# Performance work log

Measured on AMD Instinct MI355X. Metric: run time of the kernel, lower is better.

Reference implementation:

```python
import jax, jax.numpy as jnp
import numpy as np

CURVE = 1.0
TAU = 0.5
N_NODES = 32768
N_EDGES = 65536
IN_CH = 64
OUT_CH = 64
N_HEADS = 8
N_RF = 128
EPS = 1e-7


def _make_projection_matrix(m, d, seed=0):
    # FAVOR+ projection: stacked rows of transposed QR blocks, row-rescaled by chi norms.
    rng = np.random.RandomState(seed)
    blocks = []
    nb_full = m // d
    for _ in range(nb_full):
        q, _ = np.linalg.qr(rng.randn(d, d))
        blocks.append(q.T)
    rem = m - nb_full * d
    if rem > 0:
        q, _ = np.linalg.qr(rng.randn(d, d))
        blocks.append(q.T[:rem])
    final = np.vstack(blocks)  # [m, d]
    mult = np.linalg.norm(rng.randn(m, d), axis=1)
    return (mult[:, None] * final).astype(np.float32)


def _expmap0(u, c):
    # Hyperboloid exp map at origin; time slot of u is ignored.
    sqrtK = 1.0 / jnp.sqrt(c)
    x = u[..., 1:]
    xn = jnp.maximum(jnp.linalg.norm(x, axis=-1, keepdims=True), EPS)
    theta = xn / sqrtK
    return jnp.concatenate([sqrtK * jnp.cosh(theta), sqrtK * jnp.sinh(theta) * x / xn], axis=-1)


def _proj(x, c):
    # Re-project onto hyperboloid: x0 = sqrt(1/c + ||x_space||^2)
    K = 1.0 / c
    y = x[..., 1:]
    t = jnp.sqrt(K + jnp.sum(y * y, axis=-1, keepdims=True))
    return jnp.concatenate([t, y], axis=-1)


def _logmap0(x, c):
    # Hyperboloid log map at origin; output tangent has zero time component.
    sqrtK = 1.0 / jnp.sqrt(c)
    y = x[..., 1:]
    yn = jnp.maximum(jnp.linalg.norm(y, axis=-1, keepdims=True), EPS)
    t = jnp.maximum(x[..., 0:1] / sqrtK, 1.0 + EPS)
    res = sqrtK * jnp.arccosh(t) * y / yn
    return jnp.concatenate([jnp.zeros_like(res[..., :1]), res], axis=-1)


def _softmax_kernel(data, P, tau, c):
    # Performer-style exp kernel with hyperbolic (time-coordinate) prefactor.
    dt = data[..., 0:1]
    ds = data[..., 1:]
    m = 1.0 / jnp.sqrt(jnp.asarray(P.shape[0], jnp.float32))
    wx = jnp.exp(jnp.einsum('bnhd,dm->bnhm', ds, P) / jnp.sqrt(tau))
    front = jnp.exp((c / tau - dt * dt / tau) / 2.0) * m  # [b,n,h,1]
    return wx * front


def setup_inputs() -> dict:
    key = jax.random.key(0)
    k1, k2, k3, k4 = jax.random.split(key, 4)
    std = (2.0 / (IN_CH + OUT_CH)) ** 0.5
    z = 0.01 * jax.random.normal(k1, (1, N_NODES, IN_CH), jnp.float32)
    Wq = std * jax.random.normal(k2, (N_HEADS, OUT_CH, IN_CH), jnp.float32)
    Wk = std * jax.random.normal(k3, (N_HEADS, OUT_CH, IN_CH), jnp.float32)
    Wv = std * jax.random.normal(k4, (N_HEADS, OUT_CH, IN_CH), jnp.float32)
    edge_index = jax.random.randint(jax.random.fold_in(key, 7), (2, N_EDGES), 0, N_NODES, jnp.int32)
    proj_mat = jnp.asarray(_make_projection_matrix(IN_CH - 1, N_RF))  # [63, 128]
    return {"z": z, "Wq": Wq, "Wk": Wk, "Wv": Wv, "proj_mat": proj_mat, "edge_index": edge_index}


def reference(z, Wq, Wk, Wv, proj_mat, edge_index):
    c = jnp.float32(CURVE)
    tau = jnp.float32(TAU)
    zs = z[0]  # [N, C] (B == 1, squeeze)
    zh = _proj(_expmap0(zs, c), c)  # lift features to hyperboloid
    u = _logmap0(zh, c)             # [N, C], tangent at origin

    def hyplin(W):  # HypLinear (no bias): proj(expmap0(logmap0(x) @ W^T)) for all heads
        mu = jnp.einsum('nc,hoc->hno', u, W)  # [H, N, D]
        return _proj(_expmap0(mu, c), c)

    q, k, v = hyplin(Wq), hyplin(Wk), hyplin(Wv)  # [H, N, D]
    H, N, D = q.shape
    # mirrors torch stacked.reshape(-1, N, H, D) (row-major relabeling)
    query = q.reshape(1, N, H, D)
    key_ = k.reshape(1, N, H, D)
    value = v.reshape(1, N, H, D)

    qp = _softmax_kernel(query, proj_mat, tau, c).transpose(2, 0, 1, 3)  # [H,1,N,M]
    kp = _softmax_kernel(key_, proj_mat, tau, c).transpose(2, 0, 1, 3)   # [H,1,N,M]
    vv = value.transpose(2, 0, 1, 3)                                      # [H,1,N,D]

    last = jnp.einsum('hbnm,hbnd->hbmd', kp, vv)   # [H,1,M,D] kv summary
    zo = jnp.einsum('hbnm,hbmd->hbnd', qp, last)   # [H,1,N,D]
    mnorm = -zo[..., 0:1] ** 2 + jnp.sum(zo[..., 1:] ** 2, axis=-1, keepdims=True)
    zo = zo / (jnp.sqrt(c) * jnp.sqrt(jnp.abs(mnorm)))  # renormalize onto hyperboloid

    start, end = edge_index[0], edge_index[1]
    ea = jnp.einsum('hbem,hbem->hbe', qp[:, :, end, :], kp[:, :, start, :])
    A_weight = ea.transpose(1, 2, 0)  # [1, E, H]

    # hyper_agg: Euclidean head-mean followed by Minkowski renormalization
    t = jnp.mean(zo[:, 0], axis=0)  # [N, D]
    xn = -t[..., 0:1] ** 2 + jnp.sum(t[..., 1:] ** 2, axis=-1, keepdims=True)
    z_next = t / (jnp.sqrt(c) * jnp.sqrt(jnp.abs(xn)))
    link_loss = jnp.mean(A_weight)
    return z_next, link_loss
```

## Files before the change

kernel.cpp:

```cpp
#include <hip/hip_runtime.h>

#define DEV __device__ __forceinline__

#define NNODES 32768
#define NEDGES 65536
#define NROWS  262144
#define EPSF   1e-7f
#define SQRT2F 1.4142135623730951f
#define LOG2E  1.4426950408889634f
#define LOG2SQRT63 2.9886399611087573f

#define OFF_WFRAG 0u
#define OFF_LASTB 0u
#define OFF_PFRAG 196608u
#define OFF_EA    212992u
#define OFF_U     409600u
#define OFF_PART  42352640u
#define OFF_PHIQ  75907072u
#define OFF_PHIK  143015936u

typedef short s8v __attribute__((ext_vector_type(8)));
typedef float f4v __attribute__((ext_vector_type(4)));
typedef float f2v __attribute__((ext_vector_type(2)));

DEV unsigned short f2bf(float f) {
  unsigned u = __float_as_uint(f);
  return (unsigned short)((u + 0x7fffu + ((u >> 16) & 1u)) >> 16);
}
DEV float bf2f(unsigned short h) { return __uint_as_float(((unsigned)h) << 16); }
DEV unsigned pack2(float lo, float hi) {
  return __builtin_amdgcn_perm(__float_as_uint(hi) + 0x8000u, __float_as_uint(lo) + 0x8000u, 0x07060302u);
}
DEV float frcp(float x) { return __builtin_amdgcn_rcpf(x); }
DEV float fsqrt(float x) { return __builtin_amdgcn_sqrtf(x); }
DEV float fexp2(float x) { return __builtin_amdgcn_exp2f(x); }

__global__ __launch_bounds__(256) void k01_prep(const float* __restrict__ z, unsigned short* __restrict__ ubf,
                                                const float* __restrict__ Wq, const float* __restrict__ Wk,
                                                const float* __restrict__ Wv, const float* __restrict__ P,
                                                unsigned short* __restrict__ Wfrag, unsigned short* __restrict__ Pfrag,
                                                float* __restrict__ ea) {
  int i = blockIdx.x * 256 + threadIdx.x;
  float4 v = *(const float4*)(z + (size_t)i * 4);
  if ((i & 15) == 0) v.x = 0.f;
  uint2 pk;
  pk.x = pack2(v.x, v.y);
  pk.y = pack2(v.z, v.w);
  *(uint2*)(ubf + (size_t)i * 4) = pk;

  if (blockIdx.x < 96) {
    if (i == 0) ea[0] = 0.f;
    int stride = 96 * 256;
    for (int t = i; t < 98304; t += stride) {
      int j = t & 7, lane = (t >> 3) & 63, nt = (t >> 9) & 3, ks = (t >> 11) & 1, h = (t >> 12) & 7, sm = t >> 15;
      int k = ks * 32 + (lane >> 4) * 8 + j;
      int n = nt * 16 + (lane & 15);
      const float* W = (sm == 0) ? Wq : ((sm == 1) ? Wk : Wv);
      Wfrag[t] = f2bf(W[(h * 64 + n) * 64 + k]);
    }
    for (int t = i; t < 8192; t += stride) {
      int j = t & 7, lane = (t >> 3) & 63, ks = (t >> 9) & 1, mt = (t >> 10) & 7;
      int k = ks * 32 + (lane >> 4) * 8 + j;
      int r = lane & 15;
      int m = ((mt >> 2) << 6) + ((r >> 2) << 4) + ((mt & 3) << 2) + (r & 3);
      Pfrag[t] = (k == 0) ? (unsigned short)0 : f2bf(P[(k - 1) * 128 + m] * (SQRT2F * LOG2E));
    }
  }
}

__global__ __launch_bounds__(256) void k2_mfma(const unsigned short* __restrict__ ubf,
                                               const unsigned short* __restrict__ Wfrag,
                                               const unsigned short* __restrict__ Pfrag,
                                               unsigned char* __restrict__ phiq, unsigned char* __restrict__ phik,
                                               unsigned short* __restrict__ part) {
  __shared__ short lds_raw[18944];
  short* sbuf = lds_raw;
  float* sfront = (float*)(lds_raw + 18432);
  short* kbufT = lds_raw;
  short* vbufT = lds_raw + 8704;

  int w = threadIdx.x >> 6, lane = threadIdx.x & 63;
  int q = lane >> 4, l = lane & 15;
  int b = blockIdx.x;
  int h = b >> 8, t = b & 255;
  int n0 = t * 128 + w * 32;

  s8v afr[2][2];
#pragma unroll
  for (int mt = 0; mt < 2; ++mt)
#pragma unroll
    for (int ks = 0; ks < 2; ++ks)
      afr[mt][ks] = *(const s8v*)(ubf + (size_t)(n0 + mt * 16 + l) * 64 + ks * 32 + q * 8);

  const s8v* Wf = (const s8v*)Wfrag;
  const s8v* Pf = (const s8v*)Pfrag;
  uint2 vkeep[2][4];

#pragma unroll
  for (int sm = 0; sm < 3; ++sm) {
    f4v acc[2][4];
#pragma unroll
    for (int mt = 0; mt < 2; ++mt)
#pragma unroll
      for (int nt = 0; nt < 4; ++nt) acc[mt][nt] = (f4v)(0.f);
#pragma unroll
    for (int ks = 0; ks < 2; ++ks)
#pragma unroll
      for (int nt = 0; nt < 4; ++nt) {
        s8v bf = Wf[(((sm * 8 + h) * 2 + ks) * 4 + nt) * 64 + lane];
#pragma unroll
        for (int mt = 0; mt < 2; ++mt)
          acc[mt][nt] = __builtin_amdgcn_mfma_f32_16x16x32_bf16(afr[mt][ks], bf, acc[mt][nt], 0, 0, 0);
      }
#pragma unroll
    for (int mt = 0; mt < 2; ++mt) {
      float rs[4];
#pragma unroll
      for (int reg = 0; reg < 4; ++reg) {
        float v0 = (l == 0) ? 0.f : acc[mt][0][reg];
        rs[reg] = v0 * v0 + acc[mt][1][reg] * acc[mt][1][reg] + acc[mt][2][reg] * acc[mt][2][reg] +
                  acc[mt][3][reg] * acc[mt][3][reg];
      }
#pragma unroll
      for (int reg = 0; reg < 4; ++reg) {
#pragma unroll
        for (int off = 1; off < 16; off <<= 1) rs[reg] += __shfl_xor(rs[reg], off, 64);
      }
      float vreg[4][4];
#pragma unroll
      for (int reg = 0; reg < 4; ++reg) {
        float x = fmaxf(fsqrt(rs[reg]), EPSF);
        float e = fexp2(x * LOG2E);
        float sh = 0.5f * (e - frcp(e));
        float ratio = sh * frcp(x);
        float sh2 = sh * sh;
        int row = mt * 16 + q * 4 + reg;
        if (sm == 2) {
          float tt2 = fsqrt(1.f + sh2);
#pragma unroll
          for (int nt = 0; nt < 4; ++nt) {
            float val = acc[mt][nt][reg] * ratio;
            if (l == 0 && nt == 0) val = tt2;
            vreg[nt][reg] = val;
          }
        } else {
          float lf = -sh2 * LOG2E - LOG2SQRT63;
          if (l == 0) sfront[(sm * 4 + w) * 32 + row] = lf;
#pragma unroll
          for (int nt = 0; nt < 4; ++nt) {
            float val = acc[mt][nt][reg] * ratio;
            if (l == 0 && nt == 0) val = 0.f;
            sbuf[(sm * 4 + w) * 2304 + row * 72 + nt * 16 + l] = (short)(__float_as_uint(val) >> 16);
          }
        }
      }
      if (sm == 2) {
#pragma unroll
        for (int nt = 0; nt < 4; ++nt) {
          vkeep[mt][nt].x = pack2(vreg[nt][0], vreg[nt][1]);
          vkeep[mt][nt].y = pack2(vreg[nt][2], vreg[nt][3]);
        }
      }
    }
  }

  uint2 keep0[8], keep1[8];
#pragma unroll
  for (int sm = 0; sm < 2; ++sm) {
    s8v bsf[2][2];
#pragma unroll
    for (int nt = 0; nt < 2; ++nt)
#pragma unroll
      for (int ks = 0; ks < 2; ++ks)
        bsf[nt][ks] = *(const s8v*)&sbuf[(sm * 4 + w) * 2304 + (nt * 16 + l) * 72 + ks * 32 + q * 8];
    float lf0 = sfront[(sm * 4 + w) * 32 + l];
    float lf1 = sfront[(sm * 4 + w) * 32 + 16 + l];
    unsigned char* dst = sm ? phik : phiq;
    unsigned g0a[4], g0b[4], g1a[4], g1b[4];
#pragma unroll
    for (int mt = 0; mt < 8; ++mt) {
      f4v a0 = (f4v)(0.f), a1 = (f4v)(0.f);
#pragma unroll
      for (int ks = 0; ks < 2; ++ks) {
        s8v ap = Pf[(mt * 2 + ks) * 64 + lane];
        a0 = __builtin_amdgcn_mfma_f32_16x16x32_bf16(ap, bsf[0][ks], a0, 0, 0, 0);
        a1 = __builtin_amdgcn_mfma_f32_16x16x32_bf16(ap, bsf[1][ks], a1, 0, 0, 0);
      }
      float v00 = fexp2(a0[0] + lf0), v01 = fexp2(a0[1] + lf0), v02 = fexp2(a0[2] + lf0), v03 = fexp2(a0[3] + lf0);
      float v10 = fexp2(a1[0] + lf1), v11 = fexp2(a1[1] + lf1), v12 = fexp2(a1[2] + lf1), v13 = fexp2(a1[3] + lf1);
      unsigned p0 = __builtin_amdgcn_cvt_pk_fp8_f32(v00, v01, 0, 0);
      p0 = __builtin_amdgcn_cvt_pk_fp8_f32(v02, v03, p0, 1);
      unsigned p1 = __builtin_amdgcn_cvt_pk_fp8_f32(v10, v11, 0, 0);
      p1 = __builtin_amdgcn_cvt_pk_fp8_f32(v12, v13, p1, 1);
      if (mt < 4) { g0a[mt] = p0; g1a[mt] = p1; }
      else        { g0b[mt - 4] = p0; g1b[mt - 4] = p1; }
      if (sm == 1) {
        keep0[mt].x = pack2(v00, v01); keep0[mt].y = pack2(v02, v03);
        keep1[mt].x = pack2(v10, v11); keep1[mt].y = pack2(v12, v13);
      }
    }
    size_t b0 = (size_t)(n0 + l) * 1024 + (size_t)(h * 128 + q * 16);
    *(uint4*)(dst + b0)              = make_uint4(g0a[0], g0a[1], g0a[2], g0a[3]);
    *(uint4*)(dst + b0 + 64)         = make_uint4(g0b[0], g0b[1], g0b[2], g0b[3]);
    *(uint4*)(dst + b0 + 16384)      = make_uint4(g1a[0], g1a[1], g1a[2], g1a[3]);
    *(uint4*)(dst + b0 + 16384 + 64) = make_uint4(g1b[0], g1b[1], g1b[2], g1b[3]);
  }

  f4v facc[2][4];
#pragma unroll
  for (int mtl = 0; mtl < 2; ++mtl)
#pragma unroll
    for (int nt = 0; nt < 4; ++nt) facc[mtl][nt] = (f4v)(0.f);

#pragma unroll
  for (int hf = 0; hf < 2; ++hf) {
    __syncthreads();
    if ((w >> 1) == hf) {
      int nd0 = (w & 1) * 32 + l, nd1 = nd0 + 16;
#pragma unroll
      for (int mt = 0; mt < 8; ++mt) {
        int m = ((mt >> 2) << 6) + (q << 4) + ((mt & 3) << 2);
        kbufT[(m + 0) * 68 + nd0] = (short)(keep0[mt].x & 0xffffu);
        kbufT[(m + 1) * 68 + nd0] = (short)(keep0[mt].x >> 16);
        kbufT[(m + 2) * 68 + nd0] = (short)(keep0[mt].y & 0xffffu);
        kbufT[(m + 3) * 68 + nd0] = (short)(keep0[mt].y >> 16);
        kbufT[(m + 0) * 68 + nd1] = (short)(keep1[mt].x & 0xffffu);
        kbufT[(m + 1) * 68 + nd1] = (short)(keep1[mt].x >> 16);
        kbufT[(m + 2) * 68 + nd1] = (short)(keep1[mt].y & 0xffffu);
        kbufT[(m + 3) * 68 + nd1] = (short)(keep1[mt].y >> 16);
      }
#pragma unroll
      for (int mt = 0; mt < 2; ++mt)
#pragma unroll
        for (int nt = 0; nt < 4; ++nt)
          *(uint2*)&vbufT[(nt * 16 + l) * 72 + (w & 1) * 32 + mt * 16 + q * 4] = vkeep[mt][nt];
    }
    __syncthreads();
#pragma unroll
    for (int kc = 0; kc < 2; ++kc) {
      s8v bv[4];
#pragma unroll
      for (int nt = 0; nt < 4; ++nt)
        bv[nt] = *(const s8v*)&vbufT[(nt * 16 + l) * 72 + kc * 32 + q * 8];
      s8v av[2];
#pragma unroll
      for (int mtl = 0; mtl < 2; ++mtl) {
        const short* kb = &kbufT[((2 * w + mtl) * 16 + l) * 68 + kc * 32 + q * 8];
        union { s8v v; long long L[2]; } ua;
        ua.L[0] = *(const long long*)kb;
        ua.L[1] = *(const long long*)(kb + 4);
        av[mtl] = ua.v;
      }
#pragma unroll
      for (int mtl = 0; mtl < 2; ++mtl)
#pragma unroll
        for (int nt = 0; nt < 4; ++nt)
          facc[mtl][nt] = __builtin_amdgcn_mfma_f32_16x16x32_bf16(av[mtl], bv[nt], facc[mtl][nt], 0, 0, 0);
    }
  }

#pragma unroll
  for (int mtl = 0; mtl < 2; ++mtl)
#pragma unroll
    for (int nt = 0; nt < 4; ++nt) {
      uint2 pk;
      pk.x = pack2(facc[mtl][nt][0], facc[mtl][nt][1]);
      pk.y = pack2(facc[mtl][nt][2], facc[mtl][nt][3]);
      int d = nt * 16 + l;
      int m = (2 * w + mtl) * 16 + q * 4;
      *(uint2*)(part + ((size_t)((t * 8 + h) * 64 + d)) * 128 + m) = pk;
    }
}

__global__ __launch_bounds__(256) void k35(const unsigned* __restrict__ part32, unsigned char* __restrict__ lastB,
                                           const unsigned char* __restrict__ phiq,
                                           const unsigned char* __restrict__ phik,
                                           const int* __restrict__ ei, float* __restrict__ ea) {
  int b = blockIdx.x;
  if (b < 128) {
    int t2 = b * 256 + threadIdx.x;
    float s0 = 0.f, s1 = 0.f;
#pragma unroll 16
    for (int c = 0; c < 256; ++c) {
      unsigned v = part32[((size_t)c << 12) + t2];
      s0 += __uint_as_float(v << 16);
      s1 += __uint_as_float(v & 0xffff0000u);
    }
    int m = (t2 & 63) * 2, d = (t2 >> 6) & 63, h = t2 >> 12;
    int ks = m >> 5, j = m & 7, qq = (m >> 3) & 3;
    int lane = qq * 16 + (d & 15), nt = d >> 4;
    unsigned r = __builtin_amdgcn_cvt_pk_bf8_f32(s0, s1, 0, 0);
    *(unsigned short*)(lastB + ((((h * 4 + ks) * 4 + nt) * 64 + lane) << 3) + j) = (unsigned short)r;
    return;
  }
  __shared__ float part[4];
  int lane = threadIdx.x & 63, w = threadIdx.x >> 6;
  int wid = (b - 128) * 4 + w;
  float acc0 = 0.f, acc1 = 0.f;
#pragma unroll
  for (int i = 0; i < 8; i += 2) {
    int e0 = wid * 8 + i, e1 = e0 + 1;
    int s0 = ei[e0], d0 = ei[NEDGES + e0];
    int s1 = ei[e1], d1 = ei[NEDGES + e1];
    uint4 qa = *(const uint4*)(phiq + (size_t)d0 * 1024 + lane * 16);
    uint4 ka = *(const uint4*)(phik + (size_t)s0 * 1024 + lane * 16);
    uint4 qb = *(const uint4*)(phiq + (size_t)d1 * 1024 + lane * 16);
    uint4 kb = *(const uint4*)(phik + (size_t)s1 * 1024 + lane * 16);
    unsigned qs[8] = {qa.x, qa.y, qa.z, qa.w, qb.x, qb.y, qb.z, qb.w};
    unsigned ks[8] = {ka.x, ka.y, ka.z, ka.w, kb.x, kb.y, kb.z, kb.w};
#pragma unroll
    for (int p = 0; p < 8; ++p) {
      f2v q0 = __builtin_amdgcn_cvt_pk_f32_fp8(qs[p], 0);
      f2v q1 = __builtin_amdgcn_cvt_pk_f32_fp8(qs[p], 1);
      f2v k0 = __builtin_amdgcn_cvt_pk_f32_fp8(ks[p], 0);
      f2v k1 = __builtin_amdgcn_cvt_pk_f32_fp8(ks[p], 1);
      float t0 = fmaf(q0.x, k0.x, q0.y * k0.y);
      float t1 = fmaf(q1.x, k1.x, q1.y * k1.y);
      if (p < 4) acc0 += t0 + t1; else acc1 += t0 + t1;
    }
  }
  float acc = acc0 + acc1;
#pragma unroll
  for (int o = 1; o < 64; o <<= 1) acc += __shfl_xor(acc, o, 64);
  if (lane == 0) part[w] = acc;
  __syncthreads();
  if (threadIdx.x == 0) atomicAdd(ea, part[0] + part[1] + part[2] + part[3]);
}

__global__ __launch_bounds__(512) void k4_mfma(const unsigned char* __restrict__ phiq,
                                               const unsigned char* __restrict__ lastB,
                                               const float* __restrict__ ea, float* __restrict__ out) {
  __shared__ unsigned zbufT[8][64][18];
  int w = threadIdx.x >> 6, lane = threadIdx.x & 63;
  int q = lane >> 4, l = lane & 15;
  int n0 = blockIdx.x * 32;

  const long* Bf = (const long*)lastB;
  long bf[4][4];
#pragma unroll
  for (int ks = 0; ks < 4; ++ks)
#pragma unroll
    for (int nt = 0; nt < 4; ++nt) bf[ks][nt] = Bf[((w * 4 + ks) * 4 + nt) * 64 + lane];

  long af[2][4];
#pragma unroll
  for (int mt = 0; mt < 2; ++mt)
#pragma unroll
    for (int ks = 0; ks < 4; ++ks)
      af[mt][ks] = *(const long*)(phiq + (size_t)(8 * (n0 + mt * 16 + l) + w) * 128 + ks * 32 + q * 8);

  f4v acc[2][4];
#pragma unroll
  for (int mt = 0; mt < 2; ++mt)
#pragma unroll
    for (int nt = 0; nt < 4; ++nt) acc[mt][nt] = (f4v)(0.f);
#pragma unroll
  for (int ks = 0; ks < 4; ++ks)
#pragma unroll
    for (int nt = 0; nt < 4; ++nt)
#pragma unroll
      for (int mt = 0; mt < 2; ++mt)
        acc[mt][nt] = __builtin_amdgcn_mfma_f32_16x16x32_fp8_bf8(af[mt][ks], bf[ks][nt], acc[mt][nt], 0, 0, 0);

#pragma unroll
  for (int mt = 0; mt < 2; ++mt) {
    float rs[4];
#pragma unroll
    for (int reg = 0; reg < 4; ++reg) {
      float v0 = acc[mt][0][reg];
      float s0 = (l == 0) ? -v0 * v0 : v0 * v0;
      rs[reg] = s0 + acc[mt][1][reg] * acc[mt][1][reg] + acc[mt][2][reg] * acc[mt][2][reg] +
                acc[mt][3][reg] * acc[mt][3][reg];
    }
#pragma unroll
    for (int reg = 0; reg < 4; ++reg) {
#pragma unroll
      for (int off = 1; off < 16; off <<= 1) rs[reg] += __shfl_xor(rs[reg], off, 64);
    }
    float inv[4];
#pragma unroll
    for (int reg = 0; reg < 4; ++reg) inv[reg] = frcp(fsqrt(fabsf(rs[reg])));
#pragma unroll
    for (int nt = 0; nt < 4; ++nt) {
      uint2 pk;
      pk.x = pack2(acc[mt][nt][0] * inv[0], acc[mt][nt][1] * inv[1]);
      pk.y = pack2(acc[mt][nt][2] * inv[2], acc[mt][nt][3] * inv[3]);
      *(uint2*)&zbufT[w][nt * 16 + l][mt * 8 + q * 2] = pk;
    }
  }
  __syncthreads();

  int tid = threadIdx.x;
  int i = tid >> 4, dg = tid & 15;
  int i2 = i >> 1, sel = i & 1;
  float s[4] = {0.f, 0.f, 0.f, 0.f};
#pragma unroll
  for (int w2 = 0; w2 < 8; ++w2) {
#pragma unroll
    for (int j = 0; j < 4; ++j) {
      unsigned u = zbufT[w2][dg * 4 + j][i2];
      s[j] += bf2f((unsigned short)(sel ? (u >> 16) : (u & 0xffffu)));
    }
  }
  float m2 = 0.f;
#pragma unroll
  for (int j = 0; j < 4; ++j) {
    s[j] *= 0.125f;
    m2 += ((dg == 0 && j == 0) ? -s[j] * s[j] : s[j] * s[j]);
  }
#pragma unroll
  for (int off = 1; off < 16; off <<= 1) m2 += __shfl_xor(m2, off, 64);
  float inv = frcp(fsqrt(fabsf(m2)));
  float4 o = make_float4(s[0] * inv, s[1] * inv, s[2] * inv, s[3] * inv);
  *(float4*)(out + (size_t)(n0 + i) * 64 + dg * 4) = o;
  if (blockIdx.x == 0 && tid == 0) out[(size_t)NNODES * 64] = ea[0] * (1.0f / 524288.0f);
}

extern "C" void kernel_launch(void* const* d_in, const int* in_sizes, int n_in,
                              void* d_out, int out_size, void* d_ws, size_t ws_size,
                              hipStream_t stream) {
  const float* z  = (const float*)d_in[0];
  const float* Wq = (const float*)d_in[1];
  const float* Wk = (const float*)d_in[2];
  const float* Wv = (const float*)d_in[3];
  const float* P  = (const float*)d_in[4];
  const int* ei   = (const int*)d_in[5];
  char* ws = (char*)d_ws;
  unsigned short* Wfrag = (unsigned short*)(ws + OFF_WFRAG);
  unsigned char*  lastB = (unsigned char*)(ws + OFF_LASTB);
  unsigned short* Pfrag = (unsigned short*)(ws + OFF_PFRAG);
  float*          ea    = (float*)(ws + OFF_EA);
  unsigned short* ubf   = (unsigned short*)(ws + OFF_U);
  unsigned short* part  = (unsigned short*)(ws + OFF_PART);
  unsigned char*  phiq  = (unsigned char*)(ws + OFF_PHIQ);
  unsigned char*  phik  = (unsigned char*)(ws + OFF_PHIK);

  k01_prep<<<2048, 256, 0, stream>>>(z, ubf, Wq, Wk, Wv, P, Wfrag, Pfrag, ea);
  k2_mfma<<<2048, 256, 0, stream>>>(ubf, Wfrag, Pfrag, phiq, phik, part);
  k35<<<128 + 2048, 256, 0, stream>>>((const unsigned*)part, lastB, phiq, phik, ei, ea);
  k4_mfma<<<NNODES / 32, 512, 0, stream>>>(phiq, lastB, ea, (float*)d_out);
}
```

Measured before the change: 178.7 us.

## Fuse feature-map stage into projection loop and XOR-swizzle LDS tiles

Each q/k projection result is now consumed by the random-feature MFMA stage right after it is produced, inside the same loop iteration. This lets each warp reuse one staging slot instead of keeping separate q and k slots, cutting shared memory per block from about 37 KB to about 26 KB, which can allow more resident blocks per CU. XOR swizzles are added to the sbuf and kbufT row layouts to reduce LDS bank conflicts on the transposed writes and vector reads. The trade-off is more index arithmetic and possibly higher register pressure, since the keep arrays now stay live across the merged loop.

```diff
diff --git a/kernel.cpp b/kernel.cpp
--- a/kernel.cpp
+++ b/kernel.cpp
@@ -73,9 +73,9 @@
                                                const unsigned short* __restrict__ Pfrag,
                                                unsigned char* __restrict__ phiq, unsigned char* __restrict__ phik,
                                                unsigned short* __restrict__ part) {
-  __shared__ short lds_raw[18944];
+  __shared__ short lds_raw[13312];
   short* sbuf = lds_raw;
-  float* sfront = (float*)(lds_raw + 18432);
+  float* sfront = (float*)(lds_raw + 9216);
   short* kbufT = lds_raw;
   short* vbufT = lds_raw + 8704;
 
@@ -95,6 +95,7 @@
   const s8v* Wf = (const s8v*)Wfrag;
   const s8v* Pf = (const s8v*)Pfrag;
   uint2 vkeep[2][4];
+  uint2 keep0[8], keep1[8];
 
 #pragma unroll
   for (int sm = 0; sm < 3; ++sm) {
@@ -145,12 +146,13 @@
           }
         } else {
           float lf = -sh2 * LOG2E - LOG2SQRT63;
-          if (l == 0) sfront[(sm * 4 + w) * 32 + row] = lf;
+          if (l == 0) sfront[w * 32 + row] = lf;
 #pragma unroll
           for (int nt = 0; nt < 4; ++nt) {
             float val = acc[mt][nt][reg] * ratio;
             if (l == 0 && nt == 0) val = 0.f;
-            sbuf[(sm * 4 + w) * 2304 + row * 72 + nt * 16 + l] = (short)(__float_as_uint(val) >> 16);
+            sbuf[w * 2304 + row * 72 + ((nt * 16 + l) ^ ((q >> 1) << 4))] =
+                (short)(__float_as_uint(val) >> 16);
           }
         }
       }
@@ -162,48 +164,47 @@
         }
       }
     }
-  }
-
-  uint2 keep0[8], keep1[8];
-#pragma unroll
-  for (int sm = 0; sm < 2; ++sm) {
-    s8v bsf[2][2];
-#pragma unroll
-    for (int nt = 0; nt < 2; ++nt)
-#pragma unroll
-      for (int ks = 0; ks < 2; ++ks)
-        bsf[nt][ks] = *(const s8v*)&sbuf[(sm * 4 + w) * 2304 + (nt * 16 + l) * 72 + ks * 32 + q * 8];
-    float lf0 = sfront[(sm * 4 + w) * 32 + l];
-    float lf1 = sfront[(sm * 4 + w) * 32 + 16 + l];
-    unsigned char* dst = sm ? phik : phiq;
-    unsigned g0a[4], g0b[4], g1a[4], g1b[4];
-#pragma unroll
-    for (int mt = 0; mt < 8; ++mt) {
-      f4v a0 = (f4v)(0.f), a1 = (f4v)(0.f);
-#pragma unroll
-      for (int ks = 0; ks < 2; ++ks) {
-        s8v ap = Pf[(mt * 2 + ks) * 64 + lane];
-        a0 = __builtin_amdgcn_mfma_f32_16x16x32_bf16(ap, bsf[0][ks], a0, 0, 0, 0);
-        a1 = __builtin_amdgcn_mfma_f32_16x16x32_bf16(ap, bsf[1][ks], a1, 0, 0, 0);
-      }
-      float v00 = fexp2(a0[0] + lf0), v01 = fexp2(a0[1] + lf0), v02 = fexp2(a0[2] + lf0), v03 = fexp2(a0[3] + lf0);
-      float v10 = fexp2(a1[0] + lf1), v11 = fexp2(a1[1] + lf1), v12 = fexp2(a1[2] + lf1), v13 = fexp2(a1[3] + lf1);
-      unsigned p0 = __builtin_amdgcn_cvt_pk_fp8_f32(v00, v01, 0, 0);
-      p0 = __builtin_amdgcn_cvt_pk_fp8_f32(v02, v03, p0, 1);
-      unsigned p1 = __builtin_amdgcn_cvt_pk_fp8_f32(v10, v11, 0, 0);
-      p1 = __builtin_amdgcn_cvt_pk_fp8_f32(v12, v13, p1, 1);
-      if (mt < 4) { g0a[mt] = p0; g1a[mt] = p1; }
-      else        { g0b[mt - 4] = p0; g1b[mt - 4] = p1; }
-      if (sm == 1) {
-        keep0[mt].x = pack2(v00, v01); keep0[mt].y = pack2(v02, v03);
-        keep1[mt].x = pack2(v10, v11); keep1[mt].y = pack2(v12, v13);
-      }
-    }
-    size_t b0 = (size_t)(n0 + l) * 1024 + (size_t)(h * 128 + q * 16);
-    *(uint4*)(dst + b0)              = make_uint4(g0a[0], g0a[1], g0a[2], g0a[3]);
-    *(uint4*)(dst + b0 + 64)         = make_uint4(g0b[0], g0b[1], g0b[2], g0b[3]);
-    *(uint4*)(dst + b0 + 16384)      = make_uint4(g1a[0], g1a[1], g1a[2], g1a[3]);
-    *(uint4*)(dst + b0 + 16384 + 64) = make_uint4(g1b[0], g1b[1], g1b[2], g1b[3]);
+
+    if (sm < 2) {
+      int fr = (l >> 3) & 1;
+      s8v bsf[2][2];
+#pragma unroll
+      for (int nt = 0; nt < 2; ++nt)
+#pragma unroll
+        for (int ks = 0; ks < 2; ++ks)
+          bsf[nt][ks] = *(const s8v*)&sbuf[w * 2304 + (nt * 16 + l) * 72 + ((ks * 32 + q * 8) ^ (fr << 4))];
+      float lf0 = sfront[w * 32 + l];
+      float lf1 = sfront[w * 32 + 16 + l];
+      unsigned char* dst = sm ? phik : phiq;
+      unsigned g0a[4], g0b[4], g1a[4], g1b[4];
+#pragma unroll
+      for (int mt = 0; mt < 8; ++mt) {
+        f4v a0 = (f4v)(0.f), a1 = (f4v)(0.f);
+#pragma unroll
+        for (int ks = 0; ks < 2; ++ks) {
+          s8v ap = Pf[(mt * 2 + ks) * 64 + lane];
+          a0 = __builtin_amdgcn_mfma_f32_16x16x32_bf16(ap, bsf[0][ks], a0, 0, 0, 0);
+          a1 = __builtin_amdgcn_mfma_f32_16x16x32_bf16(ap, bsf[1][ks], a1, 0, 0, 0);
+        }
+        float v00 = fexp2(a0[0] + lf0), v01 = fexp2(a0[1] + lf0), v02 = fexp2(a0[2] + lf0), v03 = fexp2(a0[3] + lf0);
+        float v10 = fexp2(a1[0] + lf1), v11 = fexp2(a1[1] + lf1), v12 = fexp2(a1[2] + lf1), v13 = fexp2(a1[3] + lf1);
+        unsigned p0 = __builtin_amdgcn_cvt_pk_fp8_f32(v00, v01, 0, 0);
+        p0 = __builtin_amdgcn_cvt_pk_fp8_f32(v02, v03, p0, 1);
+        unsigned p1 = __builtin_amdgcn_cvt_pk_fp8_f32(v10, v11, 0, 0);
+        p1 = __builtin_amdgcn_cvt_pk_fp8_f32(v12, v13, p1, 1);
+        if (mt < 4) { g0a[mt] = p0; g1a[mt] = p1; }
+        else        { g0b[mt - 4] = p0; g1b[mt - 4] = p1; }
+        if (sm == 1) {
+          keep0[mt].x = pack2(v00, v01); keep0[mt].y = pack2(v02, v03);
+          keep1[mt].x = pack2(v10, v11); keep1[mt].y = pack2(v12, v13);
+        }
+      }
+      size_t b0 = (size_t)(n0 + l) * 1024 + (size_t)(h * 128 + q * 16);
+      *(uint4*)(dst + b0)              = make_uint4(g0a[0], g0a[1], g0a[2], g0a[3]);
+      *(uint4*)(dst + b0 + 64)         = make_uint4(g0b[0], g0b[1], g0b[2], g0b[3]);
+      *(uint4*)(dst + b0 + 16384)      = make_uint4(g1a[0], g1a[1], g1a[2], g1a[3]);
+      *(uint4*)(dst + b0 + 16384 + 64) = make_uint4(g1b[0], g1b[1], g1b[2], g1b[3]);
+    }
   }
 
   f4v facc[2][4];
@@ -217,17 +218,18 @@
     __syncthreads();
     if ((w >> 1) == hf) {
       int nd0 = (w & 1) * 32 + l, nd1 = nd0 + 16;
+      int c0 = nd0 ^ (q << 4), c1 = nd1 ^ (q << 4);
 #pragma unroll
       for (int mt = 0; mt < 8; ++mt) {
         int m = ((mt >> 2) << 6) + (q << 4) + ((mt & 3) << 2);
-        kbufT[(m + 0) * 68 + nd0] = (short)(keep0[mt].x & 0xffffu);
-        kbufT[(m + 1) * 68 + nd0] = (short)(keep0[mt].x >> 16);
-        kbufT[(m + 2) * 68 + nd0] = (short)(keep0[mt].y & 0xffffu);
-        kbufT[(m + 3) * 68 + nd0] = (short)(keep0[mt].y >> 16);
-        kbufT[(m + 0) * 68 + nd1] = (short)(keep1[mt].x & 0xffffu);
-        kbufT[(m + 1) * 68 + nd1] = (short)(keep1[mt].x >> 16);
-        kbufT[(m + 2) * 68 + nd1] = (short)(keep1[mt].y & 0xffffu);
-        kbufT[(m + 3) * 68 + nd1] = (short)(keep1[mt].y >> 16);
+        kbufT[(m + 0) * 68 + c0] = (short)(keep0[mt].x & 0xffffu);
+        kbufT[(m + 1) * 68 + c0] = (short)(keep0[mt].x >> 16);
+        kbufT[(m + 2) * 68 + c0] = (short)(keep0[mt].y & 0xffffu);
+        kbufT[(m + 3) * 68 + c0] = (short)(keep0[mt].y >> 16);
+        kbufT[(m + 0) * 68 + c1] = (short)(keep1[mt].x & 0xffffu);
+        kbufT[(m + 1) * 68 + c1] = (short)(keep1[mt].x >> 16);
+        kbufT[(m + 2) * 68 + c1] = (short)(keep1[mt].y & 0xffffu);
+        kbufT[(m + 3) * 68 + c1] = (short)(keep1[mt].y >> 16);
       }
 #pragma unroll
       for (int mt = 0; mt < 2; ++mt)
@@ -245,7 +247,8 @@
       s8v av[2];
 #pragma unroll
       for (int mtl = 0; mtl < 2; ++mtl) {
-        const short* kb = &kbufT[((2 * w + mtl) * 16 + l) * 68 + kc * 32 + q * 8];
+        int fr3 = (2 * w + mtl) & 3;
+        const short* kb = &kbufT[((2 * w + mtl) * 16 + l) * 68 + ((kc * 32 + q * 8) ^ (fr3 << 4))];
         union { s8v v; long long L[2]; } ua;
         ua.L[0] = *(const long long*)kb;
         ua.L[1] = *(const long long*)(kb + 4);
```

Measured after the change: 182.2 us. About the same (+1.9%).
